# Kernel optimization log

Measured on AMD Instinct MI355X. Metric: run time of the kernel, lower is better.

## Reference

```python
import jax, jax.numpy as jnp
import numpy as np

B, T, C, H, L, V = 2, 1024, 768, 12, 12, 50257
D = C // H  # head size = 64
EPS = 1e-5


def _layer_norm(x, w, b):
    m = x.mean(-1, keepdims=True)
    v = x.var(-1, keepdims=True)
    return (x - m) * jax.lax.rsqrt(v + EPS) * w + b


def setup_inputs() -> dict:
    key = jax.random.key(0)
    ks = jax.random.split(key, 8)
    std = 0.02
    res_std = 0.02 * (2 * L) ** -0.5  # NANOGPT_SCALE_INIT
    rn = lambda k, shape, s: jax.random.normal(k, shape, jnp.float32) * s
    return dict(
        idx=jax.random.randint(ks[0], (B, T), 0, V),
        wte=rn(ks[1], (V, C), std),
        wpe=rn(ks[2], (T, C), std),
        ln1_w=jnp.ones((L, C), jnp.float32), ln1_b=jnp.zeros((L, C), jnp.float32),
        qkv_w=rn(ks[3], (L, C, 3 * C), std), qkv_b=jnp.zeros((L, 3 * C), jnp.float32),
        proj_w=rn(ks[4], (L, C, C), res_std), proj_b=jnp.zeros((L, C), jnp.float32),
        ln2_w=jnp.ones((L, C), jnp.float32), ln2_b=jnp.zeros((L, C), jnp.float32),
        fc_w=rn(ks[5], (L, C, 4 * C), std), fc_b=jnp.zeros((L, 4 * C), jnp.float32),
        fco_w=rn(ks[6], (L, 4 * C, C), res_std), fco_b=jnp.zeros((L, C), jnp.float32),
        lnf_w=jnp.ones((C,), jnp.float32), lnf_b=jnp.zeros((C,), jnp.float32),
    )


def reference(idx, wte, wpe, ln1_w, ln1_b, qkv_w, qkv_b, proj_w, proj_b,
              ln2_w, ln2_b, fc_w, fc_b, fco_w, fco_b, lnf_w, lnf_b):
    x = wte[idx] + wpe[:T]  # [B, T, C] tok + pos emb
    mask = jnp.tril(jnp.ones((T, T), bool))  # causal
    scale = 1.0 / np.sqrt(D).astype(np.float32)

    def block(x, p):
        l1w, l1b, qw, qb, pw, pb, l2w, l2b, fw, fb, fow, fob = p
        h = _layer_norm(x, l1w, l1b)
        qkv = h @ qw + qb  # [B, T, 3C]
        q, k, v = jnp.split(qkv, 3, axis=-1)
        q = q.reshape(B, T, H, D)
        k = k.reshape(B, T, H, D)
        v = v.reshape(B, T, H, D)
        att = jnp.einsum('bqhd,bkhd->bhqk', q, k) * scale
        att = jnp.where(mask, att, -jnp.inf)
        att = jax.nn.softmax(att, axis=-1)
        y = jnp.einsum('bhqk,bkhd->bqhd', att, v).reshape(B, T, C)
        x = x + y @ pw + pb
        h2 = _layer_norm(x, l2w, l2b)
        x = x + jax.nn.gelu(h2 @ fw + fb, approximate=True) @ fow + fob
        return x, None

    x, _ = jax.lax.scan(block, x, (ln1_w, ln1_b, qkv_w, qkv_b, proj_w, proj_b,
                                   ln2_w, ln2_b, fc_w, fc_b, fco_w, fco_b))
    x = _layer_norm(x, lnf_w, lnf_b)
    logits = x @ wte.T  # tied lm_head
    return logits
```

## Files before the change

kernel.cpp:

```cpp
#include <hip/hip_runtime.h>
#include <cmath>
#include <cstdint>

#define T_SEQ 1024
#define NH 12
#define NL 12
#define NV 50257
#define CD 768
#define M_ROWS 2048

typedef __bf16 bf16_t;
typedef __bf16 bf16x8 __attribute__((ext_vector_type(8)));
typedef float f32x4 __attribute__((ext_vector_type(4)));

__device__ __forceinline__ void gload16(const bf16_t* g, bf16_t* l) {
  __builtin_amdgcn_global_load_lds(
      (const __attribute__((address_space(1))) void*)g,
      (__attribute__((address_space(3))) void*)l, 16, 0, 0);
}

__global__ __launch_bounds__(256) void embed_k(const int* __restrict__ idx,
    const float* __restrict__ wte, const float* __restrict__ wpe,
    float* __restrict__ x) {
  int m = blockIdx.x;
  int t = m & (T_SEQ - 1);
  int tok = idx[m];
  const float* a = wte + (size_t)tok * CD;
  const float* p = wpe + (size_t)t * CD;
  float* xr = x + (size_t)m * CD;
  int c = threadIdx.x;
  xr[c]       = a[c]       + p[c];
  xr[c + 256] = a[c + 256] + p[c + 256];
  xr[c + 512] = a[c + 512] + p[c + 512];
}

__global__ __launch_bounds__(256) void cvt_k(const float* __restrict__ in,
    bf16_t* __restrict__ out, int n4) {
  int i = blockIdx.x * 256 + threadIdx.x;
  if (i < n4) {
    float4 v = ((const float4*)in)[i];
    bf16_t* o = out + (size_t)i * 4;
    o[0] = (bf16_t)v.x; o[1] = (bf16_t)v.y;
    o[2] = (bf16_t)v.z; o[3] = (bf16_t)v.w;
  }
}

__global__ __launch_bounds__(256) void transcvt_k(const float* __restrict__ W0,
    bf16_t* __restrict__ WT0, int K, int N) {
  const float* W = W0 + (size_t)blockIdx.z * K * N;
  bf16_t* WT = WT0 + (size_t)blockIdx.z * N * K;
  __shared__ float tl[32][33];
  int k0 = blockIdx.y * 32, n0 = blockIdx.x * 32;
  int j = threadIdx.x & 31, i0 = threadIdx.x >> 5;
  #pragma unroll
  for (int i = i0; i < 32; i += 8) tl[i][j] = W[(size_t)(k0 + i) * N + n0 + j];
  __syncthreads();
  #pragma unroll
  for (int i = i0; i < 32; i += 8)
    WT[(size_t)(n0 + i) * K + k0 + j] = (bf16_t)tl[j][i];
}

__global__ __launch_bounds__(256) void ln_k(const float* __restrict__ x,
    const float* __restrict__ w, const float* __restrict__ bi,
    bf16_t* __restrict__ out) {
  int row = blockIdx.x;
  const float* xr = x + (size_t)row * CD;
  int t = threadIdx.x;
  float v0 = xr[t], v1 = xr[t + 256], v2 = xr[t + 512];
  float s = v0 + v1 + v2;
  float ss = v0 * v0 + v1 * v1 + v2 * v2;
  #pragma unroll
  for (int o = 1; o < 64; o <<= 1) { s += __shfl_xor(s, o); ss += __shfl_xor(ss, o); }
  __shared__ float sh[8];
  int wid = t >> 6, lane = t & 63;
  if (lane == 0) { sh[wid] = s; sh[4 + wid] = ss; }
  __syncthreads();
  s  = sh[0] + sh[1] + sh[2] + sh[3];
  ss = sh[4] + sh[5] + sh[6] + sh[7];
  float mean = s * (1.f / CD);
  float var  = ss * (1.f / CD) - mean * mean;
  float rs = rsqrtf(var + 1e-5f);
  bf16_t* orow = out + (size_t)row * CD;
  orow[t]       = (bf16_t)((v0 - mean) * rs * w[t]       + bi[t]);
  orow[t + 256] = (bf16_t)((v1 - mean) * rs * w[t + 256] + bi[t + 256]);
  orow[t + 512] = (bf16_t)((v2 - mean) * rs * w[t + 512] + bi[t + 512]);
}

template <int BM, int BN, int EPI>
__global__ __launch_bounds__(256) void gemm_bt(
    const bf16_t* __restrict__ A,
    const bf16_t* __restrict__ BT,
    const float* __restrict__ bias,
    const float* __restrict__ resid,
    void* __restrict__ out_p,
    int Mdim, int Ndim, int Kdim) {
  constexpr int MR = BM / 32, NR = BN / 32;
  constexpr int LPW = (BM + BN) / 64;
  __shared__ __align__(1024) bf16_t As[3][BM * 32];
  __shared__ __align__(1024) bf16_t Bs[3][BN * 32];
  const int t = threadIdx.x;
  const int wid = t >> 6, lane = t & 63;
  const int wm = wid >> 1, wn = wid & 1;
  const int m0 = blockIdx.y * BM, n0 = blockIdx.x * BN;
  const int l15 = lane & 15, lhi = lane >> 4;

  const int srow = lane >> 2;
  const int schk = lane & 3;

  auto stage = [&](int bi, int kt) {
    #pragma unroll
    for (int i = 0; i < BM / 64; ++i) {
      int rbase = wid * (BM / 4) + i * 16;
      int r = rbase + srow;
      int c = schk ^ ((r >> 1) & 3);
      gload16(A + (size_t)(m0 + r) * Kdim + kt + c * 8, &As[bi][rbase * 32]);
    }
    #pragma unroll
    for (int i = 0; i < BN / 64; ++i) {
      int rbase = wid * (BN / 4) + i * 16;
      int r = rbase + srow;
      int nr = n0 + r; if (nr >= Ndim) nr = Ndim - 1;
      int c = schk ^ ((r >> 1) & 3);
      gload16(BT + (size_t)nr * Kdim + kt + c * 8, &Bs[bi][rbase * 32]);
    }
  };

  f32x4 acc[MR][NR] = {};
  const int NT = Kdim >> 5;

  stage(0, 0);
  if (NT > 1) stage(1, 32);
  for (int tt = 0; tt < NT; ++tt) {
    if (tt < NT - 1) asm volatile("s_waitcnt vmcnt(%0)" :: "i"(LPW) : "memory");
    else             asm volatile("s_waitcnt vmcnt(0)" ::: "memory");
    __builtin_amdgcn_sched_barrier(0);
    __builtin_amdgcn_s_barrier();
    __builtin_amdgcn_sched_barrier(0);

    const bf16_t* Ab = As[tt % 3];
    const bf16_t* Bb = Bs[tt % 3];
    bf16x8 af[MR], bfr[NR];
    #pragma unroll
    for (int mm = 0; mm < MR; ++mm) {
      int ra = wm * (BM / 2) + mm * 16 + l15;
      af[mm] = *(const bf16x8*)&Ab[ra * 32 + ((lhi ^ (ra >> 1)) & 3) * 8];
    }
    #pragma unroll
    for (int nn = 0; nn < NR; ++nn) {
      int rb = wn * (BN / 2) + nn * 16 + l15;
      bfr[nn] = *(const bf16x8*)&Bb[rb * 32 + ((lhi ^ (rb >> 1)) & 3) * 8];
    }
    if (tt + 2 < NT) stage((tt + 2) % 3, (tt + 2) * 32);

    __builtin_amdgcn_s_setprio(1);
    #pragma unroll
    for (int mm = 0; mm < MR; ++mm)
      #pragma unroll
      for (int nn = 0; nn < NR; ++nn)
        acc[mm][nn] = __builtin_amdgcn_mfma_f32_16x16x32_bf16(af[mm], bfr[nn], acc[mm][nn], 0, 0, 0);
    __builtin_amdgcn_s_setprio(0);

    __builtin_amdgcn_sched_barrier(0);
    __builtin_amdgcn_s_barrier();
    __builtin_amdgcn_sched_barrier(0);
  }

  bf16_t* ob = (bf16_t*)out_p;
  float*  of = (float*)out_p;
  const int row0 = m0 + wm * (BM / 2);
  const int col0 = n0 + wn * (BN / 2);
  #pragma unroll
  for (int mm = 0; mm < MR; ++mm) {
    #pragma unroll
    for (int nn = 0; nn < NR; ++nn) {
      int col = col0 + nn * 16 + l15;
      if (col >= Ndim) continue;
      float bv = (EPI != 3) ? bias[col] : 0.f;
      #pragma unroll
      for (int r = 0; r < 4; ++r) {
        int row = row0 + mm * 16 + lhi * 4 + r;
        float v = acc[mm][nn][r] + bv;
        size_t o = (size_t)row * Ndim + col;
        if (EPI == 0) {
          ob[o] = (bf16_t)v;
        } else if (EPI == 1) {
          float u = v + 0.044715f * v * v * v;
          v = 0.5f * v * (1.f + tanhf(0.79788456080286536f * u));
          ob[o] = (bf16_t)v;
        } else if (EPI == 2) {
          of[o] = resid[o] + v;
        } else {
          of[o] = v;
        }
      }
    }
  }
}

#define LMH_GY 197
__global__ __launch_bounds__(512, 2) void gemm_lm(
    const bf16_t* __restrict__ A,
    const bf16_t* __restrict__ BT,
    float* __restrict__ out) {
  __shared__ __align__(1024) bf16_t As[4][256 * 32];
  __shared__ __align__(1024) bf16_t Bs[4][256 * 32];
  const int t = threadIdx.x;
  const int wid = t >> 6, lane = t & 63;
  const int wr = wid >> 2, wc = wid & 3;
  const int l15 = lane & 15, lhi = lane >> 4;
  const int srow = lane >> 2;
  const int schk = lane & 3;

  int lin = blockIdx.x;
  int swz = (lin & 7) * LMH_GY + (lin >> 3);
  const int m0 = (swz & 7) * 256;
  const int n0 = (swz >> 3) * 256;

  auto stage = [&](int bi, int kt) {
    #pragma unroll
    for (int hf = 0; hf < 2; ++hf) {
      int rb = hf * 128 + wid * 16;
      int r = rb + srow;
      int c = schk ^ ((r >> 1) & 3);
      gload16(A + (size_t)(m0 + r) * CD + kt * 32 + c * 8, &As[bi][rb * 32]);
    }
    #pragma unroll
    for (int hf = 0; hf < 2; ++hf) {
      int rb = hf * 128 + wid * 16;
      int r = rb + srow;
      int nr = n0 + r; if (nr >= NV) nr = NV - 1;
      int c = schk ^ ((r >> 1) & 3);
      gload16(BT + (size_t)nr * CD + kt * 32 + c * 8, &Bs[bi][rb * 32]);
    }
  };

  f32x4 acc[8][4] = {};
  const int NT = CD / 32;

  stage(0, 0); stage(1, 1); stage(2, 2);
  for (int tt = 0; tt < NT; ++tt) {
    if (tt < NT - 2)       asm volatile("s_waitcnt vmcnt(8)" ::: "memory");
    else if (tt == NT - 2) asm volatile("s_waitcnt vmcnt(4)" ::: "memory");
    else                   asm volatile("s_waitcnt vmcnt(0)" ::: "memory");
    __builtin_amdgcn_sched_barrier(0);
    __builtin_amdgcn_s_barrier();
    __builtin_amdgcn_sched_barrier(0);

    const bf16_t* Ab = As[tt & 3];
    const bf16_t* Bb = Bs[tt & 3];
    bf16x8 af[8], bfr[4];
    #pragma unroll
    for (int mm = 0; mm < 8; ++mm) {
      int ra = wr * 128 + mm * 16 + l15;
      af[mm] = *(const bf16x8*)&Ab[ra * 32 + ((lhi ^ (ra >> 1)) & 3) * 8];
    }
    #pragma unroll
    for (int nn = 0; nn < 4; ++nn) {
      int rb = wc * 64 + nn * 16 + l15;
      bfr[nn] = *(const bf16x8*)&Bb[rb * 32 + ((lhi ^ (rb >> 1)) & 3) * 8];
    }
    if (tt + 3 < NT) stage((tt + 3) & 3, tt + 3);

    __builtin_amdgcn_s_setprio(1);
    #pragma unroll
    for (int mm = 0; mm < 8; ++mm)
      #pragma unroll
      for (int nn = 0; nn < 4; ++nn)
        acc[mm][nn] = __builtin_amdgcn_mfma_f32_16x16x32_bf16(af[mm], bfr[nn], acc[mm][nn], 0, 0, 0);
    __builtin_amdgcn_s_setprio(0);

    __builtin_amdgcn_sched_barrier(0);
    __builtin_amdgcn_s_barrier();
    __builtin_amdgcn_sched_barrier(0);
  }

  const int row0 = m0 + wr * 128;
  const int col0 = n0 + wc * 64;
  #pragma unroll
  for (int mm = 0; mm < 8; ++mm) {
    #pragma unroll
    for (int nn = 0; nn < 4; ++nn) {
      int col = col0 + nn * 16 + l15;
      if (col >= NV) continue;
      #pragma unroll
      for (int r = 0; r < 4; ++r)
        out[(size_t)(row0 + mm * 16 + lhi * 4 + r) * NV + col] = acc[mm][nn][r];
    }
  }
}

__global__ __launch_bounds__(256) void vtrans_k(const bf16_t* __restrict__ qkv,
                                                bf16_t* __restrict__ VT) {
  __shared__ __align__(16) bf16_t tl[64 * 72];
  const int bh = blockIdx.y;
  const int t0 = blockIdx.x * 64;
  const int b = bh / NH, h = bh % NH;
  const int tid = threadIdx.x;
  const int row = tid >> 2;
  const int seg = (tid & 3) * 16;

  const bf16_t* src = qkv + (size_t)(b * T_SEQ + t0 + row) * (3 * CD) + 2 * CD + h * 64 + seg;
  bf16x8 v0 = *(const bf16x8*)src;
  bf16x8 v1 = *(const bf16x8*)(src + 8);
  #pragma unroll
  for (int j = 0; j < 8; ++j) tl[(seg + j) * 72 + row] = v0[j];
  #pragma unroll
  for (int j = 0; j < 8; ++j) tl[(seg + 8 + j) * 72 + row] = v1[j];
  __syncthreads();

  bf16_t* dst = VT + ((size_t)bh * 64 + row) * T_SEQ + t0 + seg;
  *(bf16x8*)dst       = *(const bf16x8*)&tl[row * 72 + seg];
  *(bf16x8*)(dst + 8) = *(const bf16x8*)&tl[row * 72 + seg + 8];
}

__global__ __launch_bounds__(64) void attn_k(const bf16_t* __restrict__ qkv,
                                             const bf16_t* __restrict__ VT,
                                             bf16_t* __restrict__ y) {
  __shared__ __align__(16) bf16_t Ps[16 * 72];
  const int lane = threadIdx.x;
  const int gw = blockIdx.x;
  const int qi = gw & 63;
  const int bh = gw >> 6;
  const int h = bh % NH, b = bh / NH;
  const bf16_t* Qbase = qkv + (size_t)b * T_SEQ * (3 * CD) + h * 64;
  const bf16_t* Kbase = Qbase + CD;
  const bf16_t* Vt = VT + (size_t)bh * 64 * T_SEQ;

  const int l15 = lane & 15, lhi = lane >> 4;
  const int q0 = qi * 16;

  bf16x8 aq[2];
  #pragma unroll
  for (int c = 0; c < 2; ++c)
    aq[c] = *(const bf16x8*)(Qbase + (size_t)(q0 + l15) * (3 * CD) + c * 32 + lhi * 8);

  f32x4 acc[4] = {};
  float m_[4], l_[4];
  #pragma unroll
  for (int r = 0; r < 4; ++r) { m_[r] = -INFINITY; l_[r] = 0.f; }

  const int qrow = q0 + lhi * 4;
  const int nt = (q0 + 79) / 64;
  for (int kt = 0; kt < nt; ++kt) {
    const int k0 = kt * 64;
    f32x4 s[4] = {};
    #pragma unroll
    for (int c = 0; c < 2; ++c) {
      #pragma unroll
      for (int kc = 0; kc < 4; ++kc) {
        bf16x8 bk = *(const bf16x8*)(Kbase + (size_t)(k0 + kc * 16 + l15) * (3 * CD) + c * 32 + lhi * 8);
        s[kc] = __builtin_amdgcn_mfma_f32_16x16x32_bf16(aq[c], bk, s[kc], 0, 0, 0);
      }
    }
    float mx[4];
    #pragma unroll
    for (int r = 0; r < 4; ++r) mx[r] = -INFINITY;
    #pragma unroll
    for (int kc = 0; kc < 4; ++kc) {
      const int kcol = k0 + kc * 16 + l15;
      #pragma unroll
      for (int r = 0; r < 4; ++r) {
        float sv = (kcol <= qrow + r) ? s[kc][r] * 0.125f : -INFINITY;
        s[kc][r] = sv;
        mx[r] = fmaxf(mx[r], sv);
      }
    }
    #pragma unroll
    for (int r = 0; r < 4; ++r) {
      mx[r] = fmaxf(mx[r], __shfl_xor(mx[r], 1));
      mx[r] = fmaxf(mx[r], __shfl_xor(mx[r], 2));
      mx[r] = fmaxf(mx[r], __shfl_xor(mx[r], 4));
      mx[r] = fmaxf(mx[r], __shfl_xor(mx[r], 8));
    }
    float al[4], rs[4];
    #pragma unroll
    for (int r = 0; r < 4; ++r) {
      float mn = fmaxf(m_[r], mx[r]);
      al[r] = __expf(m_[r] - mn);
      m_[r] = mn;
      float p0 = __expf(s[0][r] - mn);
      float p1 = __expf(s[1][r] - mn);
      float p2 = __expf(s[2][r] - mn);
      float p3 = __expf(s[3][r] - mn);
      s[0][r] = p0; s[1][r] = p1; s[2][r] = p2; s[3][r] = p3;
      rs[r] = (p0 + p1) + (p2 + p3);
    }
    #pragma unroll
    for (int r = 0; r < 4; ++r) {
      rs[r] += __shfl_xor(rs[r], 1);
      rs[r] += __shfl_xor(rs[r], 2);
      rs[r] += __shfl_xor(rs[r], 4);
      rs[r] += __shfl_xor(rs[r], 8);
      l_[r] = l_[r] * al[r] + rs[r];
    }
    #pragma unroll
    for (int dt = 0; dt < 4; ++dt)
      #pragma unroll
      for (int r = 0; r < 4; ++r) acc[dt][r] *= al[r];
    #pragma unroll
    for (int kc = 0; kc < 4; ++kc)
      #pragma unroll
      for (int r = 0; r < 4; ++r)
        Ps[(lhi * 4 + r) * 72 + kc * 16 + l15] = (bf16_t)s[kc][r];
    #pragma unroll
    for (int ks = 0; ks < 2; ++ks) {
      bf16x8 pa = *(const bf16x8*)&Ps[l15 * 72 + ks * 32 + lhi * 8];
      #pragma unroll
      for (int dt = 0; dt < 4; ++dt) {
        bf16x8 bv = *(const bf16x8*)(Vt + (size_t)(dt * 16 + l15) * T_SEQ + k0 + ks * 32 + lhi * 8);
        acc[dt] = __builtin_amdgcn_mfma_f32_16x16x32_bf16(pa, bv, acc[dt], 0, 0, 0);
      }
    }
  }
  #pragma unroll
  for (int dt = 0; dt < 4; ++dt)
    #pragma unroll
    for (int r = 0; r < 4; ++r)
      y[(size_t)(b * T_SEQ + q0 + lhi * 4 + r) * CD + h * 64 + dt * 16 + l15] =
          (bf16_t)(acc[dt][r] / l_[r]);
}

extern "C" void kernel_launch(void* const* d_in, const int* in_sizes, int n_in,
                              void* d_out, int out_size, void* d_ws, size_t ws_size,
                              hipStream_t stream) {
  const int*   idx   = (const int*)d_in[0];
  const float* wte   = (const float*)d_in[1];
  const float* wpe   = (const float*)d_in[2];
  const float* ln1w  = (const float*)d_in[3];
  const float* ln1b  = (const float*)d_in[4];
  const float* qkvw  = (const float*)d_in[5];
  const float* qkvb  = (const float*)d_in[6];
  const float* projw = (const float*)d_in[7];
  const float* projb = (const float*)d_in[8];
  const float* ln2w  = (const float*)d_in[9];
  const float* ln2b  = (const float*)d_in[10];
  const float* fcw   = (const float*)d_in[11];
  const float* fcb   = (const float*)d_in[12];
  const float* fcow  = (const float*)d_in[13];
  const float* fcob  = (const float*)d_in[14];
  const float* lnfw  = (const float*)d_in[15];
  const float* lnfb  = (const float*)d_in[16];
  float* out = (float*)d_out;

  char* w = (char*)d_ws;
  auto alloc = [&](size_t bytes) {
    char* p = w; w += (bytes + 255) & ~(size_t)255; return p;
  };
  float*  x     = (float*)alloc((size_t)M_ROWS * CD * 4);
  float*  x2    = (float*)alloc((size_t)M_ROWS * CD * 4);
  bf16_t* hb    = (bf16_t*)alloc((size_t)M_ROWS * CD * 2);
  bf16_t* qkvB  = (bf16_t*)alloc((size_t)M_ROWS * 3 * CD * 2);
  bf16_t* yb    = (bf16_t*)alloc((size_t)M_ROWS * CD * 2);
  bf16_t* fca   = (bf16_t*)alloc((size_t)M_ROWS * 4 * CD * 2);
  bf16_t* VT    = (bf16_t*)alloc((size_t)2 * NH * 64 * T_SEQ * 2);
  bf16_t* wteB  = (bf16_t*)alloc((size_t)NV * CD * 2);
  bf16_t* wqT_s = (bf16_t*)alloc((size_t)3 * CD * CD * 2);
  bf16_t* wpT_s = (bf16_t*)alloc((size_t)CD * CD * 2);
  bf16_t* wfT_s = (bf16_t*)alloc((size_t)4 * CD * CD * 2);
  bf16_t* woT_s = (bf16_t*)alloc((size_t)CD * 4 * CD * 2);
  const size_t qkvSz = (size_t)3 * CD * CD, prSz = (size_t)CD * CD;
  const size_t fcSz  = (size_t)4 * CD * CD, foSz = (size_t)CD * 4 * CD;
  bf16_t* wqT_b = (bf16_t*)alloc(NL * qkvSz * 2);
  bf16_t* wpT_b = (bf16_t*)alloc(NL * prSz * 2);
  bf16_t* wfT_b = (bf16_t*)alloc(NL * fcSz * 2);
  bf16_t* woT_b = (bf16_t*)alloc(NL * foSz * 2);
  const bool big = (size_t)(w - (char*)d_ws) <= ws_size;

  embed_k<<<M_ROWS, 256, 0, stream>>>(idx, wte, wpe, x);
  {
    int n4 = NV * CD / 4;
    cvt_k<<<(n4 + 255) / 256, 256, 0, stream>>>(wte, wteB, n4);
  }
  if (big) {
    transcvt_k<<<dim3(3 * CD / 32, CD / 32, NL), 256, 0, stream>>>(qkvw,  wqT_b, CD, 3 * CD);
    transcvt_k<<<dim3(CD / 32, CD / 32, NL),     256, 0, stream>>>(projw, wpT_b, CD, CD);
    transcvt_k<<<dim3(4 * CD / 32, CD / 32, NL), 256, 0, stream>>>(fcw,   wfT_b, CD, 4 * CD);
    transcvt_k<<<dim3(CD / 32, 4 * CD / 32, NL), 256, 0, stream>>>(fcow,  woT_b, 4 * CD, CD);
  }

  for (int l = 0; l < NL; ++l) {
    bf16_t *wqT, *wpT, *wfT, *woT;
    if (big) {
      wqT = wqT_b + (size_t)l * qkvSz; wpT = wpT_b + (size_t)l * prSz;
      wfT = wfT_b + (size_t)l * fcSz;  woT = woT_b + (size_t)l * foSz;
    } else {
      wqT = wqT_s; wpT = wpT_s; wfT = wfT_s; woT = woT_s;
      transcvt_k<<<dim3(3 * CD / 32, CD / 32, 1), 256, 0, stream>>>(qkvw  + (size_t)l * CD * 3 * CD, wqT, CD, 3 * CD);
      transcvt_k<<<dim3(CD / 32, CD / 32, 1),     256, 0, stream>>>(projw + (size_t)l * CD * CD,     wpT, CD, CD);
      transcvt_k<<<dim3(4 * CD / 32, CD / 32, 1), 256, 0, stream>>>(fcw   + (size_t)l * CD * 4 * CD, wfT, CD, 4 * CD);
      transcvt_k<<<dim3(CD / 32, 4 * CD / 32, 1), 256, 0, stream>>>(fcow  + (size_t)l * 4 * CD * CD, woT, 4 * CD, CD);
    }

    ln_k<<<M_ROWS, 256, 0, stream>>>(x, ln1w + l * CD, ln1b + l * CD, hb);
    gemm_bt<128, 128, 0><<<dim3(3 * CD / 128, M_ROWS / 128), 256, 0, stream>>>(
        hb, wqT, qkvb + l * 3 * CD, nullptr, qkvB, M_ROWS, 3 * CD, CD);
    vtrans_k<<<dim3(T_SEQ / 64, 2 * NH), 256, 0, stream>>>(qkvB, VT);
    attn_k<<<2 * NH * 64, 64, 0, stream>>>(qkvB, VT, yb);
    gemm_bt<64, 64, 2><<<dim3(CD / 64, M_ROWS / 64), 256, 0, stream>>>(
        yb, wpT, projb + l * CD, x, x2, M_ROWS, CD, CD);
    ln_k<<<M_ROWS, 256, 0, stream>>>(x2, ln2w + l * CD, ln2b + l * CD, hb);
    gemm_bt<128, 128, 1><<<dim3(4 * CD / 128, M_ROWS / 128), 256, 0, stream>>>(
        hb, wfT, fcb + l * 4 * CD, nullptr, fca, M_ROWS, 4 * CD, CD);
    gemm_bt<64, 64, 2><<<dim3(CD / 64, M_ROWS / 64), 256, 0, stream>>>(
        fca, woT, fcob + l * CD, x2, x, M_ROWS, CD, 4 * CD);
  }

  ln_k<<<M_ROWS, 256, 0, stream>>>(x, lnfw, lnfb, hb);
  gemm_lm<<<8 * LMH_GY, 512, 0, stream>>>(hb, wteB, out);
}
```

Measured before the change: 2.458 ms.

## Fuse V transpose into QKV GEMM, shrink attention key tile, add BK=64 GEMM

The QKV GEMM epilogue now writes V columns straight into the transposed VT buffer, which removes the separate vtrans kernel launch and its extra read of qkv. The attention kernel moves from 64-key tiles to 32-key tiles, so the causal diagonal wastes less work and the P scratch buffer shrinks. The GEMM gains a BK template parameter, and the fc-out GEMM (K=3072) uses BK=64 with a new swizzle to halve its k-loop iterations. In exchange, the fused epilogue issues scattered 8-byte stores, and the smaller attention tiles mean more loop iterations with more per-tile overhead.

```diff
diff --git a/kernel.cpp b/kernel.cpp
--- a/kernel.cpp
+++ b/kernel.cpp
@@ -10,6 +10,7 @@
 #define M_ROWS 2048
 
 typedef __bf16 bf16_t;
+typedef __bf16 bf16x4 __attribute__((ext_vector_type(4)));
 typedef __bf16 bf16x8 __attribute__((ext_vector_type(8)));
 typedef float f32x4 __attribute__((ext_vector_type(4)));
 
@@ -86,50 +87,69 @@
   orow[t + 512] = (bf16_t)((v2 - mean) * rs * w[t + 512] + bi[t + 512]);
 }
 
-template <int BM, int BN, int EPI>
+template <int BM, int BN, int BK, int EPI, bool FUSEVT>
 __global__ __launch_bounds__(256) void gemm_bt(
     const bf16_t* __restrict__ A,
     const bf16_t* __restrict__ BT,
     const float* __restrict__ bias,
     const float* __restrict__ resid,
     void* __restrict__ out_p,
+    bf16_t* __restrict__ vt,
     int Mdim, int Ndim, int Kdim) {
   constexpr int MR = BM / 32, NR = BN / 32;
-  constexpr int LPW = (BM + BN) / 64;
-  __shared__ __align__(1024) bf16_t As[3][BM * 32];
-  __shared__ __align__(1024) bf16_t Bs[3][BN * 32];
+  constexpr int KS = BK / 32;
+  constexpr int LPW = (BM + BN) * BK / 2048;
+  __shared__ __align__(1024) bf16_t As[3][BM * BK];
+  __shared__ __align__(1024) bf16_t Bs[3][BN * BK];
   const int t = threadIdx.x;
   const int wid = t >> 6, lane = t & 63;
   const int wm = wid >> 1, wn = wid & 1;
   const int m0 = blockIdx.y * BM, n0 = blockIdx.x * BN;
   const int l15 = lane & 15, lhi = lane >> 4;
 
-  const int srow = lane >> 2;
-  const int schk = lane & 3;
-
   auto stage = [&](int bi, int kt) {
-    #pragma unroll
-    for (int i = 0; i < BM / 64; ++i) {
-      int rbase = wid * (BM / 4) + i * 16;
-      int r = rbase + srow;
-      int c = schk ^ ((r >> 1) & 3);
-      gload16(A + (size_t)(m0 + r) * Kdim + kt + c * 8, &As[bi][rbase * 32]);
-    }
-    #pragma unroll
-    for (int i = 0; i < BN / 64; ++i) {
-      int rbase = wid * (BN / 4) + i * 16;
-      int r = rbase + srow;
-      int nr = n0 + r; if (nr >= Ndim) nr = Ndim - 1;
-      int c = schk ^ ((r >> 1) & 3);
-      gload16(BT + (size_t)nr * Kdim + kt + c * 8, &Bs[bi][rbase * 32]);
+    if (BK == 32) {
+      const int srow = lane >> 2, schk = lane & 3;
+      #pragma unroll
+      for (int i = 0; i < BM / 64; ++i) {
+        int rbase = wid * (BM / 4) + i * 16;
+        int r = rbase + srow;
+        int c = schk ^ ((r >> 1) & 3);
+        gload16(A + (size_t)(m0 + r) * Kdim + kt + c * 8, &As[bi][rbase * 32]);
+      }
+      #pragma unroll
+      for (int i = 0; i < BN / 64; ++i) {
+        int rbase = wid * (BN / 4) + i * 16;
+        int r = rbase + srow;
+        int nr = n0 + r; if (nr >= Ndim) nr = Ndim - 1;
+        int c = schk ^ ((r >> 1) & 3);
+        gload16(BT + (size_t)nr * Kdim + kt + c * 8, &Bs[bi][rbase * 32]);
+      }
+    } else {
+      const int srow = lane >> 3, schk = lane & 7;
+      #pragma unroll
+      for (int i = 0; i < BM / 32; ++i) {
+        int rbase = wid * (BM / 4) + i * 8;
+        int r = rbase + srow;
+        int c = schk ^ (r & 7);
+        gload16(A + (size_t)(m0 + r) * Kdim + kt + c * 8, &As[bi][rbase * 64]);
+      }
+      #pragma unroll
+      for (int i = 0; i < BN / 32; ++i) {
+        int rbase = wid * (BN / 4) + i * 8;
+        int r = rbase + srow;
+        int nr = n0 + r; if (nr >= Ndim) nr = Ndim - 1;
+        int c = schk ^ (r & 7);
+        gload16(BT + (size_t)nr * Kdim + kt + c * 8, &Bs[bi][rbase * 64]);
+      }
     }
   };
 
   f32x4 acc[MR][NR] = {};
-  const int NT = Kdim >> 5;
+  const int NT = Kdim / BK;
 
   stage(0, 0);
-  if (NT > 1) stage(1, 32);
+  if (NT > 1) stage(1, BK);
   for (int tt = 0; tt < NT; ++tt) {
     if (tt < NT - 1) asm volatile("s_waitcnt vmcnt(%0)" :: "i"(LPW) : "memory");
     else             asm volatile("s_waitcnt vmcnt(0)" ::: "memory");
@@ -139,25 +159,33 @@
 
     const bf16_t* Ab = As[tt % 3];
     const bf16_t* Bb = Bs[tt % 3];
-    bf16x8 af[MR], bfr[NR];
-    #pragma unroll
-    for (int mm = 0; mm < MR; ++mm) {
-      int ra = wm * (BM / 2) + mm * 16 + l15;
-      af[mm] = *(const bf16x8*)&Ab[ra * 32 + ((lhi ^ (ra >> 1)) & 3) * 8];
-    }
-    #pragma unroll
-    for (int nn = 0; nn < NR; ++nn) {
-      int rb = wn * (BN / 2) + nn * 16 + l15;
-      bfr[nn] = *(const bf16x8*)&Bb[rb * 32 + ((lhi ^ (rb >> 1)) & 3) * 8];
-    }
-    if (tt + 2 < NT) stage((tt + 2) % 3, (tt + 2) * 32);
+    bf16x8 af[KS][MR], bfr[KS][NR];
+    #pragma unroll
+    for (int ks = 0; ks < KS; ++ks) {
+      #pragma unroll
+      for (int mm = 0; mm < MR; ++mm) {
+        int ra = wm * (BM / 2) + mm * 16 + l15;
+        int ch = (BK == 32) ? ((lhi ^ (ra >> 1)) & 3) : ((ks * 4 + lhi) ^ (ra & 7));
+        af[ks][mm] = *(const bf16x8*)&Ab[ra * BK + ch * 8];
+      }
+      #pragma unroll
+      for (int nn = 0; nn < NR; ++nn) {
+        int rb = wn * (BN / 2) + nn * 16 + l15;
+        int ch = (BK == 32) ? ((lhi ^ (rb >> 1)) & 3) : ((ks * 4 + lhi) ^ (rb & 7));
+        bfr[ks][nn] = *(const bf16x8*)&Bb[rb * BK + ch * 8];
+      }
+    }
+    if (tt + 2 < NT) stage((tt + 2) % 3, (tt + 2) * BK);
 
     __builtin_amdgcn_s_setprio(1);
     #pragma unroll
-    for (int mm = 0; mm < MR; ++mm)
-      #pragma unroll
-      for (int nn = 0; nn < NR; ++nn)
-        acc[mm][nn] = __builtin_amdgcn_mfma_f32_16x16x32_bf16(af[mm], bfr[nn], acc[mm][nn], 0, 0, 0);
+    for (int ks = 0; ks < KS; ++ks)
+      #pragma unroll
+      for (int mm = 0; mm < MR; ++mm)
+        #pragma unroll
+        for (int nn = 0; nn < NR; ++nn)
+          acc[mm][nn] = __builtin_amdgcn_mfma_f32_16x16x32_bf16(
+              af[ks][mm], bfr[ks][nn], acc[mm][nn], 0, 0, 0);
     __builtin_amdgcn_s_setprio(0);
 
     __builtin_amdgcn_sched_barrier(0);
@@ -176,21 +204,38 @@
       int col = col0 + nn * 16 + l15;
       if (col >= Ndim) continue;
       float bv = (EPI != 3) ? bias[col] : 0.f;
-      #pragma unroll
-      for (int r = 0; r < 4; ++r) {
-        int row = row0 + mm * 16 + lhi * 4 + r;
-        float v = acc[mm][nn][r] + bv;
-        size_t o = (size_t)row * Ndim + col;
-        if (EPI == 0) {
-          ob[o] = (bf16_t)v;
-        } else if (EPI == 1) {
-          float u = v + 0.044715f * v * v * v;
-          v = 0.5f * v * (1.f + tanhf(0.79788456080286536f * u));
-          ob[o] = (bf16_t)v;
-        } else if (EPI == 2) {
-          of[o] = resid[o] + v;
-        } else {
-          of[o] = v;
+      if (EPI == 0) {
+        bf16_t vv[4];
+        #pragma unroll
+        for (int r = 0; r < 4; ++r) {
+          int row = row0 + mm * 16 + lhi * 4 + r;
+          float v = acc[mm][nn][r] + bv;
+          vv[r] = (bf16_t)v;
+          ob[(size_t)row * Ndim + col] = vv[r];
+        }
+        if (FUSEVT && col >= 2 * CD) {
+          int h = (col - 2 * CD) >> 6;
+          int d = (col - 2 * CD) & 63;
+          int brow = row0 + mm * 16 + lhi * 4;
+          int bh = (brow >> 10) * NH + h;
+          int tt0 = brow & (T_SEQ - 1);
+          *(bf16x4*)&vt[((size_t)bh * 64 + d) * T_SEQ + tt0] = *(const bf16x4*)vv;
+        }
+      } else {
+        #pragma unroll
+        for (int r = 0; r < 4; ++r) {
+          int row = row0 + mm * 16 + lhi * 4 + r;
+          float v = acc[mm][nn][r] + bv;
+          size_t o = (size_t)row * Ndim + col;
+          if (EPI == 1) {
+            float u = v + 0.044715f * v * v * v;
+            v = 0.5f * v * (1.f + tanhf(0.79788456080286536f * u));
+            ob[o] = (bf16_t)v;
+          } else if (EPI == 2) {
+            of[o] = resid[o] + v;
+          } else {
+            of[o] = v;
+          }
         }
       }
     }
@@ -289,34 +334,10 @@
   }
 }
 
-__global__ __launch_bounds__(256) void vtrans_k(const bf16_t* __restrict__ qkv,
-                                                bf16_t* __restrict__ VT) {
-  __shared__ __align__(16) bf16_t tl[64 * 72];
-  const int bh = blockIdx.y;
-  const int t0 = blockIdx.x * 64;
-  const int b = bh / NH, h = bh % NH;
-  const int tid = threadIdx.x;
-  const int row = tid >> 2;
-  const int seg = (tid & 3) * 16;
-
-  const bf16_t* src = qkv + (size_t)(b * T_SEQ + t0 + row) * (3 * CD) + 2 * CD + h * 64 + seg;
-  bf16x8 v0 = *(const bf16x8*)src;
-  bf16x8 v1 = *(const bf16x8*)(src + 8);
-  #pragma unroll
-  for (int j = 0; j < 8; ++j) tl[(seg + j) * 72 + row] = v0[j];
-  #pragma unroll
-  for (int j = 0; j < 8; ++j) tl[(seg + 8 + j) * 72 + row] = v1[j];
-  __syncthreads();
-
-  bf16_t* dst = VT + ((size_t)bh * 64 + row) * T_SEQ + t0 + seg;
-  *(bf16x8*)dst       = *(const bf16x8*)&tl[row * 72 + seg];
-  *(bf16x8*)(dst + 8) = *(const bf16x8*)&tl[row * 72 + seg + 8];
-}
-
 __global__ __launch_bounds__(64) void attn_k(const bf16_t* __restrict__ qkv,
                                              const bf16_t* __restrict__ VT,
                                              bf16_t* __restrict__ y) {
-  __shared__ __align__(16) bf16_t Ps[16 * 72];
+  __shared__ __align__(16) bf16_t Ps[16 * 40];
   const int lane = threadIdx.x;
   const int gw = blockIdx.x;
   const int qi = gw & 63;
@@ -340,14 +361,14 @@
   for (int r = 0; r < 4; ++r) { m_[r] = -INFINITY; l_[r] = 0.f; }
 
   const int qrow = q0 + lhi * 4;
-  const int nt = (q0 + 79) / 64;
+  const int nt = (q0 + 47) / 32;
   for (int kt = 0; kt < nt; ++kt) {
-    const int k0 = kt * 64;
-    f32x4 s[4] = {};
+    const int k0 = kt * 32;
+    f32x4 s[2] = {};
     #pragma unroll
     for (int c = 0; c < 2; ++c) {
       #pragma unroll
-      for (int kc = 0; kc < 4; ++kc) {
+      for (int kc = 0; kc < 2; ++kc) {
         bf16x8 bk = *(const bf16x8*)(Kbase + (size_t)(k0 + kc * 16 + l15) * (3 * CD) + c * 32 + lhi * 8);
         s[kc] = __builtin_amdgcn_mfma_f32_16x16x32_bf16(aq[c], bk, s[kc], 0, 0, 0);
       }
@@ -356,7 +377,7 @@
     #pragma unroll
     for (int r = 0; r < 4; ++r) mx[r] = -INFINITY;
     #pragma unroll
-    for (int kc = 0; kc < 4; ++kc) {
+    for (int kc = 0; kc < 2; ++kc) {
       const int kcol = k0 + kc * 16 + l15;
       #pragma unroll
       for (int r = 0; r < 4; ++r) {
@@ -380,10 +401,8 @@
       m_[r] = mn;
       float p0 = __expf(s[0][r] - mn);
       float p1 = __expf(s[1][r] - mn);
-      float p2 = __expf(s[2][r] - mn);
-      float p3 = __expf(s[3][r] - mn);
-      s[0][r] = p0; s[1][r] = p1; s[2][r] = p2; s[3][r] = p3;
-      rs[r] = (p0 + p1) + (p2 + p3);
+      s[0][r] = p0; s[1][r] = p1;
+      rs[r] = p0 + p1;
     }
     #pragma unroll
     for (int r = 0; r < 4; ++r) {
@@ -398,18 +417,15 @@
       #pragma unroll
       for (int r = 0; r < 4; ++r) acc[dt][r] *= al[r];
     #pragma unroll
-    for (int kc = 0; kc < 4; ++kc)
+    for (int kc = 0; kc < 2; ++kc)
       #pragma unroll
       for (int r = 0; r < 4; ++r)
-        Ps[(lhi * 4 + r) * 72 + kc * 16 + l15] = (bf16_t)s[kc][r];
-    #pragma unroll
-    for (int ks = 0; ks < 2; ++ks) {
-      bf16x8 pa = *(const bf16x8*)&Ps[l15 * 72 + ks * 32 + lhi * 8];
-      #pragma unroll
-      for (int dt = 0; dt < 4; ++dt) {
-        bf16x8 bv = *(const bf16x8*)(Vt + (size_t)(dt * 16 + l15) * T_SEQ + k0 + ks * 32 + lhi * 8);
-        acc[dt] = __builtin_amdgcn_mfma_f32_16x16x32_bf16(pa, bv, acc[dt], 0, 0, 0);
-      }
+        Ps[(lhi * 4 + r) * 40 + kc * 16 + l15] = (bf16_t)s[kc][r];
+    bf16x8 pa = *(const bf16x8*)&Ps[l15 * 40 + lhi * 8];
+    #pragma unroll
+    for (int dt = 0; dt < 4; ++dt) {
+      bf16x8 bv = *(const bf16x8*)(Vt + (size_t)(dt * 16 + l15) * T_SEQ + k0 + lhi * 8);
+      acc[dt] = __builtin_amdgcn_mfma_f32_16x16x32_bf16(pa, bv, acc[dt], 0, 0, 0);
     }
   }
   #pragma unroll
@@ -492,17 +508,16 @@
     }
 
     ln_k<<<M_ROWS, 256, 0, stream>>>(x, ln1w + l * CD, ln1b + l * CD, hb);
-    gemm_bt<128, 128, 0><<<dim3(3 * CD / 128, M_ROWS / 128), 256, 0, stream>>>(
-        hb, wqT, qkvb + l * 3 * CD, nullptr, qkvB, M_ROWS, 3 * CD, CD);
-    vtrans_k<<<dim3(T_SEQ / 64, 2 * NH), 256, 0, stream>>>(qkvB, VT);
+    gemm_bt<128, 128, 32, 0, true><<<dim3(3 * CD / 128, M_ROWS / 128), 256, 0, stream>>>(
+        hb, wqT, qkvb + l * 3 * CD, nullptr, qkvB, VT, M_ROWS, 3 * CD, CD);
     attn_k<<<2 * NH * 64, 64, 0, stream>>>(qkvB, VT, yb);
-    gemm_bt<64, 64, 2><<<dim3(CD / 64, M_ROWS / 64), 256, 0, stream>>>(
-        yb, wpT, projb + l * CD, x, x2, M_ROWS, CD, CD);
+    gemm_bt<64, 64, 32, 2, false><<<dim3(CD / 64, M_ROWS / 64), 256, 0, stream>>>(
+        yb, wpT, projb + l * CD, x, x2, nullptr, M_ROWS, CD, CD);
     ln_k<<<M_ROWS, 256, 0, stream>>>(x2, ln2w + l * CD, ln2b + l * CD, hb);
-    gemm_bt<128, 128, 1><<<dim3(4 * CD / 128, M_ROWS / 128), 256, 0, stream>>>(
-        hb, wfT, fcb + l * 4 * CD, nullptr, fca, M_ROWS, 4 * CD, CD);
-    gemm_bt<64, 64, 2><<<dim3(CD / 64, M_ROWS / 64), 256, 0, stream>>>(
-        fca, woT, fcob + l * CD, x2, x, M_ROWS, CD, 4 * CD);
+    gemm_bt<128, 128, 32, 1, false><<<dim3(4 * CD / 128, M_ROWS / 128), 256, 0, stream>>>(
+        hb, wfT, fcb + l * 4 * CD, nullptr, fca, nullptr, M_ROWS, 4 * CD, CD);
+    gemm_bt<64, 64, 64, 2, false><<<dim3(CD / 64, M_ROWS / 64), 256, 0, stream>>>(
+        fca, woT, fcob + l * CD, x2, x, nullptr, M_ROWS, CD, 4 * CD);
   }
 
   ln_k<<<M_ROWS, 256, 0, stream>>>(x, lnfw, lnfb, hb);
```

Result: faster. 2.178 ms (-11.4%).
